# Performance work log

Measured on AMD Instinct MI355X. Metric: run time of the kernel, lower is better.

## Reference

```python
import jax, jax.numpy as jnp
import numpy as np
from jax import lax

# ---- static config (R-C3D TEST cfg) ----
FEAT_STRIDE = 8
SCALES = np.array([2, 4, 5, 6, 8, 9, 10, 12, 14, 16], dtype=np.float32)
NUM_ANCHORS = SCALES.shape[0]  # A = 10
PRE_NMS_TOP_N = 6000
POST_NMS_TOP_N = 300
NMS_THRESH = 0.7
MIN_SIZE = 8.0


def _generate_anchors():
    # matches generate_anchors(base_size=feat_stride, scales): centered temporal windows
    ctr = (FEAT_STRIDE - 1) / 2.0
    ws = SCALES * FEAT_STRIDE
    return np.stack([ctr - 0.5 * (ws - 1.0), ctr + 0.5 * (ws - 1.0)], axis=1).astype(np.float32)  # [A,2]


def setup_inputs() -> dict:
    key = jax.random.key(0)
    k1, k2 = jax.random.split(key)
    B, L = 4, 4096
    scores_in = jax.random.normal(k1, (B, 2 * NUM_ANCHORS, L, 1, 1), dtype=jnp.float32)
    twin_deltas = jax.random.normal(k2, (B, 2 * NUM_ANCHORS, L, 1, 1), dtype=jnp.float32) * 0.1
    return {"scores_in": scores_in, "twin_deltas": twin_deltas}


def _iou_1d(twins):
    # twins: [N,2] inclusive temporal segments (torch-style +1 lengths)
    x1, x2 = twins[:, 0], twins[:, 1]
    length = x2 - x1 + 1.0
    inter = jnp.maximum(0.0, jnp.minimum(x2[:, None], x2[None, :]) - jnp.maximum(x1[:, None], x1[None, :]) + 1.0)
    union = length[:, None] + length[None, :] - inter
    return inter / union


def _nms_keep(iou, thresh):
    # greedy NMS on score-sorted candidates; keep[i] iff no earlier kept j overlaps > thresh
    N = iou.shape[0]
    idx = jnp.arange(N)
    def body(i, keep):
        suppressed = jnp.any(keep & (iou[:, i] > thresh) & (idx < i))
        return keep.at[i].set(~suppressed)
    return lax.fori_loop(0, N, body, jnp.zeros((N,), dtype=bool))


def _forward(scores_in, twin_deltas):
    B = scores_in.shape[0]
    A = NUM_ANCHORS
    L = scores_in.shape[2]
    anchors0 = jnp.asarray(_generate_anchors())  # [A,2]

    # objectness scores: second half of channels
    scores = scores_in[:, A:, :, :, :]  # [B,A,L,1,1]

    # shifted anchors, shift-major / anchor-minor to match (L,H,W,A) flattening
    shifts = jnp.arange(L, dtype=scores_in.dtype) * FEAT_STRIDE  # [L]
    anc = (anchors0[None, :, :] + shifts[:, None, None]).reshape(L * A, 2)  # [K*A,2]

    deltas = jnp.transpose(twin_deltas, (0, 2, 3, 4, 1)).reshape(B, -1, 2)  # [B,K*A,2]
    sc = jnp.transpose(scores, (0, 2, 3, 4, 1)).reshape(B, -1)  # [B,K*A]

    # twin_transform_inv
    widths = anc[:, 1] - anc[:, 0] + 1.0  # [K*A]
    ctr = anc[:, 0] + 0.5 * widths
    pred_ctr = deltas[:, :, 0] * widths[None, :] + ctr[None, :]
    pred_l = jnp.exp(deltas[:, :, 1]) * widths[None, :]
    proposals = jnp.stack([pred_ctr - 0.5 * pred_l, pred_ctr + 0.5 * pred_l], axis=-1)  # [B,K*A,2]

    # clip_twins to [0, L*feat_stride - 1]
    proposals = jnp.clip(proposals, 0.0, L * FEAT_STRIDE - 1.0)

    # filter: zero scores of too-short proposals
    ls = proposals[:, :, 1] - proposals[:, :, 0] + 1.0
    sc = jnp.where(ls < MIN_SIZE, 0.0, sc)

    # sort by score descending, take pre-NMS top-N
    order = jnp.argsort(-sc, axis=1)[:, :PRE_NMS_TOP_N]  # [B,P]
    prop_sorted = jnp.take_along_axis(proposals, order[:, :, None], axis=1)  # [B,P,2]

    def per_image(p):
        iou = _iou_1d(lax.stop_gradient(p))  # NMS decision is non-differentiable (layer propagates no grads via NMS)
        keep = _nms_keep(iou, NMS_THRESH)
        N = p.shape[0]
        # kept indices in sorted order, padded with N
        kept_idx = jnp.sort(jnp.where(keep, jnp.arange(N), N))[:POST_NMS_TOP_N]
        valid = kept_idx < N
        gi = jnp.minimum(kept_idx, N - 1)
        return jnp.where(valid[:, None], p[gi], 0.0)  # [post,2]

    props_out = jax.vmap(per_image)(prop_sorted)  # [B,post,2]
    batch_ids = jnp.broadcast_to(
        jnp.arange(B, dtype=scores_in.dtype)[:, None, None], (B, POST_NMS_TOP_N, 1)
    )
    return jnp.concatenate([batch_ids, props_out], axis=-1)  # [B,post,3]


def reference(scores_in, twin_deltas):
    return _forward(scores_in, twin_deltas)
```

## Files before the change

### kernel.cpp

```cpp
#include <hip/hip_runtime.h>
#include <stdint.h>

#pragma clang fp contract(off)

#define NA 10
#define LL 4096
#define NB 4
#define NSEL (LL * NA)
#define PRE2 2048
#define POST_NMS 300
#define CAND 4096
#define NHB12 4096
#define TWORDS 33792

__constant__ float c_WS[NA] = {16.f, 32.f, 40.f, 48.f, 64.f, 72.f, 80.f, 96.f, 112.f, 128.f};

__device__ inline void gload_lds16(const void* g, void* l) {
    __builtin_amdgcn_global_load_lds(
        (const __attribute__((address_space(1))) unsigned*)g,
        (__attribute__((address_space(3))) unsigned*)l, 16, 0, 0);
}

__global__ __launch_bounds__(1024) void k_prep(const float* __restrict__ scores,
                                               const float* __restrict__ deltas,
                                               unsigned long long* __restrict__ packed,
                                               float2* __restrict__ prop,
                                               unsigned* __restrict__ hpart) {
    __shared__ unsigned shist[NHB12];
    const int tid = threadIdx.x;
    const int a = blockIdx.x;
    const int b = blockIdx.y;

    #pragma unroll
    for (int i = 0; i < 4; ++i) shist[i * 1024 + tid] = 0;
    __syncthreads();

    const float4 s4  = ((const float4*)scores)[((b * 20 + 10 + a) << 10) + tid];
    const float4 d04 = ((const float4*)deltas)[((b * 20 + 2 * a) << 10) + tid];
    const float4 d14 = ((const float4*)deltas)[((b * 20 + 2 * a + 1) << 10) + tid];
    const float w = c_WS[a];
    const int l0 = tid << 2;
    const int r = (a << 12) + l0;

    unsigned key[4];
    float x1v[4], x2v[4];
    #pragma unroll
    for (int k = 0; k < 4; ++k) {
        const float d0 = (k == 0) ? d04.x : (k == 1) ? d04.y : (k == 2) ? d04.z : d04.w;
        const float d1 = (k == 0) ? d14.x : (k == 1) ? d14.y : (k == 2) ? d14.z : d14.w;
        float sv      = (k == 0) ? s4.x  : (k == 1) ? s4.y  : (k == 2) ? s4.z  : s4.w;
        const float ctr = (float)(8 * (l0 + k) + 4);
        const float pc = d0 * w + ctr;
        const float pl = expf(d1) * w;
        const float x1 = fminf(fmaxf(pc - 0.5f * pl, 0.0f), 32767.0f);
        const float x2 = fminf(fmaxf(pc + 0.5f * pl, 0.0f), 32767.0f);
        if (x2 - x1 + 1.0f < 8.0f) sv = 0.0f;
        const unsigned u = __float_as_uint(sv);
        key[k] = (u & 0x80000000u) ? ~u : (u | 0x80000000u);
        x1v[k] = x1; x2v[k] = x2;
    }
    const unsigned long long p0 = ((unsigned long long)key[0] << 32) | (unsigned)(0xFFFFFFFFu - (unsigned)((l0 + 0) * NA + a));
    const unsigned long long p1 = ((unsigned long long)key[1] << 32) | (unsigned)(0xFFFFFFFFu - (unsigned)((l0 + 1) * NA + a));
    const unsigned long long p2 = ((unsigned long long)key[2] << 32) | (unsigned)(0xFFFFFFFFu - (unsigned)((l0 + 2) * NA + a));
    const unsigned long long p3 = ((unsigned long long)key[3] << 32) | (unsigned)(0xFFFFFFFFu - (unsigned)((l0 + 3) * NA + a));
    *(ulonglong2*)&packed[b * NSEL + r]     = make_ulonglong2(p0, p1);
    *(ulonglong2*)&packed[b * NSEL + r + 2] = make_ulonglong2(p2, p3);
    *(float4*)&prop[b * NSEL + r]     = make_float4(x1v[0], x2v[0], x1v[1], x2v[1]);
    *(float4*)&prop[b * NSEL + r + 2] = make_float4(x1v[2], x2v[2], x1v[3], x2v[3]);

    #pragma unroll
    for (int k = 0; k < 4; ++k) atomicAdd(&shist[key[k] >> 20], 1u);
    __syncthreads();

    ((uint4*)&hpart[(b * 10 + a) << 12])[tid] = ((const uint4*)shist)[tid];
}

__global__ __launch_bounds__(1024, 1) void k_select(const unsigned long long* __restrict__ packed,
                                                    const unsigned* __restrict__ hpart,
                                                    unsigned long long* __restrict__ cand,
                                                    int* __restrict__ gcnt) {
    __shared__ unsigned swsum[16];
    __shared__ unsigned skmin;
    __shared__ int sCnt;

    const int tid = threadIdx.x;
    const int lane = tid & 63;
    const int wv = tid >> 6;
    const int b = blockIdx.x;

    if (tid == 0) sCnt = 0;

    uint4 h = make_uint4(0, 0, 0, 0);
    #pragma unroll
    for (int c = 0; c < 10; ++c) {
        const uint4 v = ((const uint4*)hpart)[((b * 10 + c) << 10) + tid];
        h.x += v.x; h.y += v.y; h.z += v.z; h.w += v.w;
    }
    const unsigned s = h.x + h.y + h.z + h.w;

    unsigned inc = s;
    #pragma unroll
    for (int d = 1; d < 64; d <<= 1) {
        unsigned u = (unsigned)__shfl_down((int)inc, d, 64);
        if (lane + d < 64) inc += u;
    }
    if (lane == 0) swsum[wv] = inc;
    __syncthreads();
    if (tid < 16) {
        unsigned t = swsum[tid];
        unsigned winc = t;
        #pragma unroll
        for (int d = 1; d < 16; d <<= 1) {
            unsigned u = (unsigned)__shfl_down((int)winc, d, 64);
            if (tid + d < 16) winc += u;
        }
        swsum[tid] = winc - t;
    }
    __syncthreads();

    {
        const unsigned glob = inc + swsum[wv];
        const unsigned base = glob - s;
        const unsigned t3 = base + h.w;
        const unsigned t2 = t3 + h.z;
        const unsigned t1 = t2 + h.y;
        const unsigned t0 = t1 + h.x;
        const unsigned bx = (unsigned)(tid << 2);
        if (t0 >= (unsigned)PRE2 && t0 - h.x < (unsigned)PRE2) skmin = (bx + 0) << 20;
        if (t1 >= (unsigned)PRE2 && t1 - h.y < (unsigned)PRE2) skmin = (bx + 1) << 20;
        if (t2 >= (unsigned)PRE2 && t2 - h.z < (unsigned)PRE2) skmin = (bx + 2) << 20;
        if (t3 >= (unsigned)PRE2 && t3 - h.w < (unsigned)PRE2) skmin = (bx + 3) << 20;
    }
    __syncthreads();
    const unsigned kmin = skmin;

    const unsigned long long* pk = packed + b * NSEL;
    ulonglong2 pf[4];
    #pragma unroll
    for (int i = 0; i < 4; ++i) pf[i] = *(const ulonglong2*)&pk[((i * 1024 + tid) << 1)];
    #pragma unroll
    for (int it = 0; it < NSEL / 2048; ++it) {
        const ulonglong2 pp = pf[it & 3];
        if (it + 4 < NSEL / 2048)
            pf[it & 3] = *(const ulonglong2*)&pk[(((it + 4) * 1024 + tid) << 1)];
        const bool pd0 = ((unsigned)(pp.x >> 32) >= kmin);
        const bool pd1 = ((unsigned)(pp.y >> 32) >= kmin);
        const unsigned long long m0 = __ballot(pd0);
        const unsigned long long m1 = __ballot(pd1);
        const int cnt = (int)(__popcll(m0) + __popcll(m1));
        int base = 0;
        if (cnt) {
            if (lane == 0) base = atomicAdd(&sCnt, cnt);
            base = __shfl(base, 0, 64);
            const unsigned long long below = (1ULL << lane) - 1ULL;
            if (pd0) {
                int pos = base + (int)__popcll(m0 & below);
                if (pos < CAND) cand[b * CAND + pos] = pp.x;
            }
            if (pd1) {
                int pos = base + (int)__popcll(m0) + (int)__popcll(m1 & below);
                if (pos < CAND) cand[b * CAND + pos] = pp.y;
            }
        }
    }
    __syncthreads();
    if (tid == 0) gcnt[b] = sCnt;
}

__global__ __launch_bounds__(256) void k_rank(const unsigned long long* __restrict__ cand,
                                              const int* __restrict__ gcnt,
                                              const float2* __restrict__ prop,
                                              float2* __restrict__ srt) {
    __shared__ __align__(16) unsigned long long keys[CAND];
    __shared__ unsigned part[4][64][4];

    const int b = blockIdx.y;
    const int n0 = gcnt[b];
    const int n = n0 < CAND ? n0 : CAND;
    const int ib = blockIdx.x * 256;
    if (ib >= n) return;

    const int tid = threadIdx.x;
    const int lane = tid & 63;
    const int wv = tid >> 6;
    const unsigned long long* cb = cand + b * CAND;

    const int nP = (n + 7) & ~7;
    for (int j = tid; j < nP; j += 256)
        keys[j] = (j < n) ? cb[j] : 0ULL;
    __syncthreads();

    const int i0 = ib + (lane << 2);
    const unsigned long long k0 = keys[i0 + 0];
    const unsigned long long k1 = keys[i0 + 1];
    const unsigned long long k2 = keys[i0 + 2];
    const unsigned long long k3 = keys[i0 + 3];

    const int q = nP >> 2;
    const ulonglong2* keys2 = (const ulonglong2*)keys;
    const int p0 = (wv * q) >> 1;
    const int pn = q >> 1;
    unsigned r0 = 0, r1 = 0, r2 = 0, r3 = 0;
    #pragma unroll 4
    for (int p = 0; p < pn; ++p) {
        ulonglong2 kj = keys2[p0 + p];
        r0 += (kj.x > k0); r0 += (kj.y > k0);
        r1 += (kj.x > k1); r1 += (kj.y > k1);
        r2 += (kj.x > k2); r2 += (kj.y > k2);
        r3 += (kj.x > k3); r3 += (kj.y > k3);
    }
    part[wv][lane][0] = r0; part[wv][lane][1] = r1;
    part[wv][lane][2] = r2; part[wv][lane][3] = r3;
    __syncthreads();

    const int ig = ib + tid;
    if (ig < n) {
        const int l_ = tid >> 2, c_ = tid & 3;
        unsigned r = part[0][l_][c_] + part[1][l_][c_] + part[2][l_][c_] + part[3][l_][c_];
        if (r < PRE2) {
            unsigned long long k = keys[ig];
            unsigned idx_ = 0xFFFFFFFFu - (unsigned)k;
            unsigned a_ = idx_ % 10u, l2_ = idx_ / 10u;
            srt[b * PRE2 + r] = prop[b * NSEL + (a_ << 12) + l2_];
        }
    }
}

__global__ __launch_bounds__(256) void k_mask(const float2* __restrict__ srt,
                                              unsigned long long* __restrict__ maskT) {
    const int g  = blockIdx.x;
    const int wj = blockIdx.y;
    const int b  = blockIdx.z;
    if (g * 4 > wj) return;

    __shared__ float2 lj[256];
    const int tid = threadIdx.x;
    lj[tid] = srt[b * PRE2 + (g << 8) + tid];
    __syncthreads();

    const int wi = (g << 2) + (tid >> 6);
    if (wi > wj) return;
    const int j = (wj << 6) + (tid & 63);

    float2 pj = srt[b * PRE2 + j];
    float ljn = pj.y - pj.x + 1.0f;
    unsigned long long bits = 0ULL;
    const int lbase = (tid >> 6) * 64;
    const int ibase = wi << 6;
    #pragma unroll 4
    for (int t = 0; t < 64; ++t) {
        float2 pv = lj[lbase + t];
        float inter = fminf(pj.y, pv.y) - fmaxf(pj.x, pv.x) + 1.0f;
        bool sup = false;
        if (inter > 0.0f) {
            float uni = ljn + (pv.y - pv.x + 1.0f) - inter;
            sup = (inter / uni) > 0.7f;
        }
        if ((ibase + t < j) && sup) bits |= (1ULL << t);
    }
    maskT[(size_t)b * TWORDS + (size_t)((wj * (wj + 1) / 2) + wi) * 64 + (tid & 63)] = bits;
}

__global__ __launch_bounds__(64, 1) void k_reduce(const unsigned long long* __restrict__ maskT,
                                                  const float2* __restrict__ srt,
                                                  float* __restrict__ out) {
    const int b = blockIdx.x;
    const int lane = threadIdx.x;
    __shared__ unsigned long long colbuf[4][2048];
    __shared__ unsigned long long Kl[32];
    __shared__ int sKl[POST_NMS];

    const unsigned long long* mTb = maskT + (size_t)b * TWORDS;

    auto stage = [&](int wv, int buf) {
        const char* src = (const char*)(mTb + (size_t)(wv * (wv + 1) / 2) * 64) + lane * 16;
        char* dst = (char*)(&colbuf[buf][0]);
        #pragma unroll
        for (int k = 0; k < 16; ++k)
            gload_lds16(src + k * 1024, dst + k * 1024);
    };

    stage(0, 0); stage(1, 1); stage(2, 2); stage(3, 3);

    int kept = 0;
    bool done = false;

    for (int w = 0; w < 32 && !done; ++w) {
        asm volatile("s_waitcnt vmcnt(48)" ::: "memory");
        __builtin_amdgcn_sched_barrier(0);

        const unsigned long long* cw = &colbuf[w & 3][0];
        unsigned long long SUP = 0ULL;
        for (int wi = 0; wi < w; ++wi)
            SUP |= Kl[wi] & cw[(wi << 6) + lane];
        unsigned long long x = cw[(w << 6) + lane];

        unsigned long long avail = ~__ballot(SUP != 0ULL);
        asm volatile("s_waitcnt lgkmcnt(0)" ::: "memory");
        __builtin_amdgcn_sched_barrier(0);
        asm volatile("" : "+v"(x));
        {
            int nx = w + 4;
            stage(nx < 31 ? nx : 31, nx & 3);
        }

        unsigned long long keptw = 0ULL;
        while (avail) {
            int j = __ffsll((long long)avail) - 1;
            if (lane == 0) sKl[kept] = (w << 6) + j;
            kept++; keptw |= (1ULL << j);
            if (kept >= POST_NMS) { done = true; break; }
            unsigned long long supb = __ballot(((x >> j) & 1ULL) != 0ULL);
            avail &= ~supb;
            avail &= ~(1ULL << j);
        }
        if (lane == 0) Kl[w] = keptw;
    }

    __syncthreads();
    for (int t = lane; t < POST_NMS; t += 64) {
        float x1 = 0.0f, x2 = 0.0f;
        if (t < kept) {
            float2 pv = srt[b * PRE2 + sKl[t]];
            x1 = pv.x; x2 = pv.y;
        }
        float* o = out + (size_t)(b * POST_NMS + t) * 3;
        o[0] = (float)b; o[1] = x1; o[2] = x2;
    }
}

extern "C" void kernel_launch(void* const* d_in, const int* in_sizes, int n_in,
                              void* d_out, int out_size, void* d_ws, size_t ws_size,
                              hipStream_t stream) {
    const float* scores = (const float*)d_in[0];
    const float* deltas = (const float*)d_in[1];
    float* out = (float*)d_out;

    char* ws = (char*)d_ws;
    unsigned long long* packed = (unsigned long long*)ws;
    float2* prop = (float2*)(ws + 1310720);
    float2* srt  = (float2*)(ws + 2621440);
    unsigned long long* maskT = (unsigned long long*)(ws + 2686976);
    unsigned long long* cand  = (unsigned long long*)(ws + 3768320);
    int* gcnt                 = (int*)(ws + 3899392);
    unsigned* hpart           = (unsigned*)(ws + 3899408);

    k_prep<<<dim3(NA, NB), 1024, 0, stream>>>(scores, deltas, packed, prop, hpart);
    k_select<<<NB, 1024, 0, stream>>>(packed, hpart, cand, gcnt);
    k_rank<<<dim3(CAND / 256, NB), 256, 0, stream>>>(cand, gcnt, prop, srt);
    k_mask<<<dim3(8, 32, NB), 256, 0, stream>>>(srt, maskT);
    k_reduce<<<NB, 64, 0, stream>>>(maskT, srt, out);
}
```

Before: 77.80 us.

## Fuse candidate selection into rank kernel, recomputing threshold per block

Removes the separate k_select launch. Each k_rank block now sums the histogram partials, finds the score threshold, and does a deterministic two-pass count-and-compact of the 40960 packed keys straight into shared memory. This saves one kernel launch and the global cand/gcnt round trip. In exchange, all 16 blocks per image redundantly rescan the packed keys twice, and blocks with ib>=n still do the full scan.

Result: slower. 98.21 us (+26.2%).

```diff
diff --git a/kernel.cpp b/kernel.cpp
--- a/kernel.cpp
+++ b/kernel.cpp
@@ -75,153 +75,130 @@
     ((uint4*)&hpart[(b * 10 + a) << 12])[tid] = ((const uint4*)shist)[tid];
 }
 
-__global__ __launch_bounds__(1024, 1) void k_select(const unsigned long long* __restrict__ packed,
-                                                    const unsigned* __restrict__ hpart,
-                                                    unsigned long long* __restrict__ cand,
-                                                    int* __restrict__ gcnt) {
-    __shared__ unsigned swsum[16];
-    __shared__ unsigned skmin;
-    __shared__ int sCnt;
-
-    const int tid = threadIdx.x;
-    const int lane = tid & 63;
-    const int wv = tid >> 6;
-    const int b = blockIdx.x;
-
-    if (tid == 0) sCnt = 0;
-
-    uint4 h = make_uint4(0, 0, 0, 0);
-    #pragma unroll
-    for (int c = 0; c < 10; ++c) {
-        const uint4 v = ((const uint4*)hpart)[((b * 10 + c) << 10) + tid];
-        h.x += v.x; h.y += v.y; h.z += v.z; h.w += v.w;
-    }
-    const unsigned s = h.x + h.y + h.z + h.w;
-
-    unsigned inc = s;
-    #pragma unroll
-    for (int d = 1; d < 64; d <<= 1) {
-        unsigned u = (unsigned)__shfl_down((int)inc, d, 64);
-        if (lane + d < 64) inc += u;
-    }
-    if (lane == 0) swsum[wv] = inc;
-    __syncthreads();
-    if (tid < 16) {
-        unsigned t = swsum[tid];
-        unsigned winc = t;
-        #pragma unroll
-        for (int d = 1; d < 16; d <<= 1) {
-            unsigned u = (unsigned)__shfl_down((int)winc, d, 64);
-            if (tid + d < 16) winc += u;
-        }
-        swsum[tid] = winc - t;
-    }
-    __syncthreads();
-
-    {
-        const unsigned glob = inc + swsum[wv];
-        const unsigned base = glob - s;
-        const unsigned t3 = base + h.w;
-        const unsigned t2 = t3 + h.z;
-        const unsigned t1 = t2 + h.y;
-        const unsigned t0 = t1 + h.x;
-        const unsigned bx = (unsigned)(tid << 2);
-        if (t0 >= (unsigned)PRE2 && t0 - h.x < (unsigned)PRE2) skmin = (bx + 0) << 20;
-        if (t1 >= (unsigned)PRE2 && t1 - h.y < (unsigned)PRE2) skmin = (bx + 1) << 20;
-        if (t2 >= (unsigned)PRE2 && t2 - h.z < (unsigned)PRE2) skmin = (bx + 2) << 20;
-        if (t3 >= (unsigned)PRE2 && t3 - h.w < (unsigned)PRE2) skmin = (bx + 3) << 20;
-    }
-    __syncthreads();
-    const unsigned kmin = skmin;
-
-    const unsigned long long* pk = packed + b * NSEL;
-    ulonglong2 pf[4];
-    #pragma unroll
-    for (int i = 0; i < 4; ++i) pf[i] = *(const ulonglong2*)&pk[((i * 1024 + tid) << 1)];
-    #pragma unroll
-    for (int it = 0; it < NSEL / 2048; ++it) {
-        const ulonglong2 pp = pf[it & 3];
-        if (it + 4 < NSEL / 2048)
-            pf[it & 3] = *(const ulonglong2*)&pk[(((it + 4) * 1024 + tid) << 1)];
-        const bool pd0 = ((unsigned)(pp.x >> 32) >= kmin);
-        const bool pd1 = ((unsigned)(pp.y >> 32) >= kmin);
-        const unsigned long long m0 = __ballot(pd0);
-        const unsigned long long m1 = __ballot(pd1);
-        const int cnt = (int)(__popcll(m0) + __popcll(m1));
-        int base = 0;
-        if (cnt) {
-            if (lane == 0) base = atomicAdd(&sCnt, cnt);
-            base = __shfl(base, 0, 64);
-            const unsigned long long below = (1ULL << lane) - 1ULL;
-            if (pd0) {
-                int pos = base + (int)__popcll(m0 & below);
-                if (pos < CAND) cand[b * CAND + pos] = pp.x;
-            }
-            if (pd1) {
-                int pos = base + (int)__popcll(m0) + (int)__popcll(m1 & below);
-                if (pos < CAND) cand[b * CAND + pos] = pp.y;
-            }
-        }
-    }
-    __syncthreads();
-    if (tid == 0) gcnt[b] = sCnt;
-}
-
-__global__ __launch_bounds__(256) void k_rank(const unsigned long long* __restrict__ cand,
-                                              const int* __restrict__ gcnt,
+__global__ __launch_bounds__(256) void k_rank(const unsigned long long* __restrict__ packed,
+                                              const unsigned* __restrict__ hpart,
                                               const float2* __restrict__ prop,
                                               float2* __restrict__ srt) {
     __shared__ __align__(16) unsigned long long keys[CAND];
     __shared__ unsigned part[4][64][4];
-
-    const int b = blockIdx.y;
-    const int n0 = gcnt[b];
-    const int n = n0 < CAND ? n0 : CAND;
-    const int ib = blockIdx.x * 256;
-    if (ib >= n) return;
+    __shared__ unsigned swsum[4];
+    __shared__ int scnt[4];
+    __shared__ unsigned skmin;
 
     const int tid = threadIdx.x;
     const int lane = tid & 63;
     const int wv = tid >> 6;
-    const unsigned long long* cb = cand + b * CAND;
-
+    const int b = blockIdx.y;
+    const int ib = blockIdx.x * 256;
+
+    unsigned h[16];
+    {
+        #pragma unroll
+        for (int k = 0; k < 16; ++k) h[k] = 0;
+        #pragma unroll
+        for (int c = 0; c < 10; ++c) {
+            const uint4* hp = (const uint4*)&hpart[((b * 10 + c) << 12) + (tid << 4)];
+            #pragma unroll
+            for (int q = 0; q < 4; ++q) {
+                const uint4 v = hp[q];
+                h[q * 4 + 0] += v.x; h[q * 4 + 1] += v.y;
+                h[q * 4 + 2] += v.z; h[q * 4 + 3] += v.w;
+            }
+        }
+    }
+    unsigned s = 0;
+    #pragma unroll
+    for (int k = 0; k < 16; ++k) s += h[k];
+
+    {
+        unsigned inc = s;
+        #pragma unroll
+        for (int d = 1; d < 64; d <<= 1) {
+            unsigned u = (unsigned)__shfl_down((int)inc, d, 64);
+            if (lane + d < 64) inc += u;
+        }
+        if (lane == 0) swsum[wv] = inc;
+        __syncthreads();
+        unsigned after = 0;
+        for (int w2 = wv + 1; w2 < 4; ++w2) after += swsum[w2];
+        const unsigned glob = inc + after;
+        unsigned cum = glob - s;
+        #pragma unroll
+        for (int k = 15; k >= 0; --k) {
+            cum += h[k];
+            if (cum >= (unsigned)PRE2 && (cum - h[k]) < (unsigned)PRE2)
+                skmin = ((unsigned)((tid << 4) + k)) << 20;
+        }
+    }
+    __syncthreads();
+    const unsigned kmin = skmin;
+
+    const unsigned long long* pk = packed + b * NSEL;
+    int cnt = 0;
+    #pragma unroll 8
+    for (int i = 0; i < 160; ++i)
+        cnt += (int)((unsigned)(pk[i * 256 + tid] >> 32) >= kmin);
+
+    int incp = cnt;
+    #pragma unroll
+    for (int d = 1; d < 64; d <<= 1) {
+        int u = __shfl_up(incp, d, 64);
+        if (lane >= d) incp += u;
+    }
+    if (lane == 63) scnt[wv] = incp;
+    __syncthreads();
+    int waveoff = 0;
+    for (int w2 = 0; w2 < wv; ++w2) waveoff += scnt[w2];
+    int pos = waveoff + incp - cnt;
+    int n = scnt[0] + scnt[1] + scnt[2] + scnt[3];
+    if (n > CAND) n = CAND;
     const int nP = (n + 7) & ~7;
-    for (int j = tid; j < nP; j += 256)
-        keys[j] = (j < n) ? cb[j] : 0ULL;
-    __syncthreads();
-
-    const int i0 = ib + (lane << 2);
-    const unsigned long long k0 = keys[i0 + 0];
-    const unsigned long long k1 = keys[i0 + 1];
-    const unsigned long long k2 = keys[i0 + 2];
-    const unsigned long long k3 = keys[i0 + 3];
-
-    const int q = nP >> 2;
-    const ulonglong2* keys2 = (const ulonglong2*)keys;
-    const int p0 = (wv * q) >> 1;
-    const int pn = q >> 1;
-    unsigned r0 = 0, r1 = 0, r2 = 0, r3 = 0;
+
     #pragma unroll 4
-    for (int p = 0; p < pn; ++p) {
-        ulonglong2 kj = keys2[p0 + p];
-        r0 += (kj.x > k0); r0 += (kj.y > k0);
-        r1 += (kj.x > k1); r1 += (kj.y > k1);
-        r2 += (kj.x > k2); r2 += (kj.y > k2);
-        r3 += (kj.x > k3); r3 += (kj.y > k3);
-    }
-    part[wv][lane][0] = r0; part[wv][lane][1] = r1;
-    part[wv][lane][2] = r2; part[wv][lane][3] = r3;
-    __syncthreads();
-
-    const int ig = ib + tid;
-    if (ig < n) {
-        const int l_ = tid >> 2, c_ = tid & 3;
-        unsigned r = part[0][l_][c_] + part[1][l_][c_] + part[2][l_][c_] + part[3][l_][c_];
-        if (r < PRE2) {
-            unsigned long long k = keys[ig];
-            unsigned idx_ = 0xFFFFFFFFu - (unsigned)k;
-            unsigned a_ = idx_ % 10u, l2_ = idx_ / 10u;
-            srt[b * PRE2 + r] = prop[b * NSEL + (a_ << 12) + l2_];
+    for (int i = 0; i < 160; ++i) {
+        const unsigned long long e = pk[i * 256 + tid];
+        if ((unsigned)(e >> 32) >= kmin) {
+            if (pos < CAND) keys[pos] = e;
+            ++pos;
+        }
+    }
+    for (int j = n + tid; j < nP; j += 256) keys[j] = 0ULL;
+    __syncthreads();
+
+    if (ib < n) {
+        const int i0 = ib + (lane << 2);
+        const unsigned long long k0 = keys[i0 + 0];
+        const unsigned long long k1 = keys[i0 + 1];
+        const unsigned long long k2 = keys[i0 + 2];
+        const unsigned long long k3 = keys[i0 + 3];
+
+        const int q = nP >> 2;
+        const ulonglong2* keys2 = (const ulonglong2*)keys;
+        const int p0 = (wv * q) >> 1;
+        const int pn = q >> 1;
+        unsigned r0 = 0, r1 = 0, r2 = 0, r3 = 0;
+        #pragma unroll 4
+        for (int p = 0; p < pn; ++p) {
+            ulonglong2 kj = keys2[p0 + p];
+            r0 += (kj.x > k0); r0 += (kj.y > k0);
+            r1 += (kj.x > k1); r1 += (kj.y > k1);
+            r2 += (kj.x > k2); r2 += (kj.y > k2);
+            r3 += (kj.x > k3); r3 += (kj.y > k3);
+        }
+        part[wv][lane][0] = r0; part[wv][lane][1] = r1;
+        part[wv][lane][2] = r2; part[wv][lane][3] = r3;
+        __syncthreads();
+
+        const int ig = ib + tid;
+        if (ig < n) {
+            const int l_ = tid >> 2, c_ = tid & 3;
+            unsigned r = part[0][l_][c_] + part[1][l_][c_] + part[2][l_][c_] + part[3][l_][c_];
+            if (r < PRE2) {
+                unsigned long long k = keys[ig];
+                unsigned idx_ = 0xFFFFFFFFu - (unsigned)k;
+                unsigned a_ = idx_ % 10u, l2_ = idx_ / 10u;
+                srt[b * PRE2 + r] = prop[b * NSEL + (a_ << 12) + l2_];
+            }
         }
     }
 }
@@ -341,13 +318,10 @@
     float2* prop = (float2*)(ws + 1310720);
     float2* srt  = (float2*)(ws + 2621440);
     unsigned long long* maskT = (unsigned long long*)(ws + 2686976);
-    unsigned long long* cand  = (unsigned long long*)(ws + 3768320);
-    int* gcnt                 = (int*)(ws + 3899392);
     unsigned* hpart           = (unsigned*)(ws + 3899408);
 
     k_prep<<<dim3(NA, NB), 1024, 0, stream>>>(scores, deltas, packed, prop, hpart);
-    k_select<<<NB, 1024, 0, stream>>>(packed, hpart, cand, gcnt);
-    k_rank<<<dim3(CAND / 256, NB), 256, 0, stream>>>(cand, gcnt, prop, srt);
+    k_rank<<<dim3(CAND / 256, NB), 256, 0, stream>>>(packed, hpart, prop, srt);
     k_mask<<<dim3(8, 32, NB), 256, 0, stream>>>(srt, maskT);
     k_reduce<<<NB, 64, 0, stream>>>(maskT, srt, out);
 }
```

## Split candidate selection across 10 blocks per image with global atomic compaction

Applied to the files above, without the earlier changes.

k_select previously ran one 1024-thread block per image, streaming all 40960 packed keys. It now launches 10 blocks per image, each handling 4096 keys. Each block computes its own threshold from the histogram, does a block-level prefix count, and reserves output space with one global atomicAdd on gcnt, which k_prep now zeroes. This raises parallelism from 4 blocks to 40. The cost is that every block repeats the histogram reduction and scan, and candidate order across blocks becomes nondeterministic, which k_rank must tolerate.

Result: faster. 71.52 us (-8.1%).

```diff
diff --git a/kernel.cpp b/kernel.cpp
--- a/kernel.cpp
+++ b/kernel.cpp
@@ -25,11 +25,14 @@
                                                const float* __restrict__ deltas,
                                                unsigned long long* __restrict__ packed,
                                                float2* __restrict__ prop,
-                                               unsigned* __restrict__ hpart) {
+                                               unsigned* __restrict__ hpart,
+                                               int* __restrict__ gcnt) {
     __shared__ unsigned shist[NHB12];
     const int tid = threadIdx.x;
     const int a = blockIdx.x;
     const int b = blockIdx.y;
+
+    if (a == 0 && tid == 0) gcnt[b] = 0;
 
     #pragma unroll
     for (int i = 0; i < 4; ++i) shist[i * 1024 + tid] = 0;
@@ -81,14 +84,13 @@
                                                     int* __restrict__ gcnt) {
     __shared__ unsigned swsum[16];
     __shared__ unsigned skmin;
-    __shared__ int sCnt;
+    __shared__ int wcnt[16];
+    __shared__ int sbase;
 
     const int tid = threadIdx.x;
     const int lane = tid & 63;
     const int wv = tid >> 6;
-    const int b = blockIdx.x;
-
-    if (tid == 0) sCnt = 0;
+    const int b = blockIdx.y;
 
     uint4 h = make_uint4(0, 0, 0, 0);
     #pragma unroll
@@ -117,7 +119,6 @@
         swsum[tid] = winc - t;
     }
     __syncthreads();
-
     {
         const unsigned glob = inc + swsum[wv];
         const unsigned base = glob - s;
@@ -134,37 +135,36 @@
     __syncthreads();
     const unsigned kmin = skmin;
 
-    const unsigned long long* pk = packed + b * NSEL;
-    ulonglong2 pf[4];
-    #pragma unroll
-    for (int i = 0; i < 4; ++i) pf[i] = *(const ulonglong2*)&pk[((i * 1024 + tid) << 1)];
-    #pragma unroll
-    for (int it = 0; it < NSEL / 2048; ++it) {
-        const ulonglong2 pp = pf[it & 3];
-        if (it + 4 < NSEL / 2048)
-            pf[it & 3] = *(const ulonglong2*)&pk[(((it + 4) * 1024 + tid) << 1)];
-        const bool pd0 = ((unsigned)(pp.x >> 32) >= kmin);
-        const bool pd1 = ((unsigned)(pp.y >> 32) >= kmin);
-        const unsigned long long m0 = __ballot(pd0);
-        const unsigned long long m1 = __ballot(pd1);
-        const int cnt = (int)(__popcll(m0) + __popcll(m1));
-        int base = 0;
-        if (cnt) {
-            if (lane == 0) base = atomicAdd(&sCnt, cnt);
-            base = __shfl(base, 0, 64);
-            const unsigned long long below = (1ULL << lane) - 1ULL;
-            if (pd0) {
-                int pos = base + (int)__popcll(m0 & below);
-                if (pos < CAND) cand[b * CAND + pos] = pp.x;
-            }
-            if (pd1) {
-                int pos = base + (int)__popcll(m0) + (int)__popcll(m1 & below);
-                if (pos < CAND) cand[b * CAND + pos] = pp.y;
-            }
-        }
-    }
-    __syncthreads();
-    if (tid == 0) gcnt[b] = sCnt;
+    const unsigned long long* pk = packed + b * NSEL + (blockIdx.x << 12);
+    const ulonglong2 e0 = ((const ulonglong2*)pk)[tid];
+    const ulonglong2 e1 = ((const ulonglong2*)pk)[1024 + tid];
+
+    const bool pa = ((unsigned)(e0.x >> 32) >= kmin);
+    const bool pb = ((unsigned)(e0.y >> 32) >= kmin);
+    const bool pc = ((unsigned)(e1.x >> 32) >= kmin);
+    const bool pd = ((unsigned)(e1.y >> 32) >= kmin);
+    const unsigned long long ma = __ballot(pa);
+    const unsigned long long mb = __ballot(pb);
+    const unsigned long long mc = __ballot(pc);
+    const unsigned long long md = __ballot(pd);
+    const int ca = (int)__popcll(ma), cb2 = (int)__popcll(mb);
+    const int cc = (int)__popcll(mc), cd = (int)__popcll(md);
+    if (lane == 0) wcnt[wv] = ca + cb2 + cc + cd;
+    __syncthreads();
+    if (tid == 0) {
+        int t = 0;
+        #pragma unroll
+        for (int w2 = 0; w2 < 16; ++w2) { int v = wcnt[w2]; wcnt[w2] = t; t += v; }
+        sbase = atomicAdd(&gcnt[b], t);
+    }
+    __syncthreads();
+    const int base = sbase + wcnt[wv];
+    const unsigned long long below = (1ULL << lane) - 1ULL;
+    unsigned long long* cb = cand + b * CAND;
+    if (pa) { int p = base + (int)__popcll(ma & below);                 if (p < CAND) cb[p] = e0.x; }
+    if (pb) { int p = base + ca + (int)__popcll(mb & below);            if (p < CAND) cb[p] = e0.y; }
+    if (pc) { int p = base + ca + cb2 + (int)__popcll(mc & below);      if (p < CAND) cb[p] = e1.x; }
+    if (pd) { int p = base + ca + cb2 + cc + (int)__popcll(md & below); if (p < CAND) cb[p] = e1.y; }
 }
 
 __global__ __launch_bounds__(256) void k_rank(const unsigned long long* __restrict__ cand,
@@ -345,8 +345,8 @@
     int* gcnt                 = (int*)(ws + 3899392);
     unsigned* hpart           = (unsigned*)(ws + 3899408);
 
-    k_prep<<<dim3(NA, NB), 1024, 0, stream>>>(scores, deltas, packed, prop, hpart);
-    k_select<<<NB, 1024, 0, stream>>>(packed, hpart, cand, gcnt);
+    k_prep<<<dim3(NA, NB), 1024, 0, stream>>>(scores, deltas, packed, prop, hpart, gcnt);
+    k_select<<<dim3(10, NB), 1024, 0, stream>>>(packed, hpart, cand, gcnt);
     k_rank<<<dim3(CAND / 256, NB), 256, 0, stream>>>(cand, gcnt, prop, srt);
     k_mask<<<dim3(8, 32, NB), 256, 0, stream>>>(srt, maskT);
     k_reduce<<<NB, 64, 0, stream>>>(maskT, srt, out);
```
